# Kernel optimization log

Hardware: AMD Instinct MI355X
Metric: run time of the kernel (lower is better)

The kernel has to match this reference:

```python
import jax, jax.numpy as jnp
import numpy as np

B, L, E = 512, 64, 1024
D_MODEL, H = 1024, 16
HD = D_MODEL // H  # 64
SMOL_CH, SMOL_HID, SMOL_GEN = 32, 256, 256
LN_EPS = 1e-3


def _layernorm(x, g, b, eps=LN_EPS):
    m = jnp.mean(x, axis=-1, keepdims=True)
    v = jnp.mean(jnp.square(x - m), axis=-1, keepdims=True)
    return (x - m) * jax.lax.rsqrt(v + eps) * g + b


def setup_inputs() -> dict:
    key = jax.random.key(0)
    ks = jax.random.split(key, 12)
    s = lambda fan_in: 1.0 / np.sqrt(fan_in)
    inp = {
        'x': jax.random.normal(ks[0], (B, L, E), dtype=jnp.float32),
        # attention projections (stored as [in, out])
        'wq': jax.random.normal(ks[1], (E, D_MODEL), dtype=jnp.float32) * s(E),
        'bq': jnp.zeros((D_MODEL,), jnp.float32),
        'wk': jax.random.normal(ks[2], (E, D_MODEL), dtype=jnp.float32) * s(E),
        'bk': jnp.zeros((D_MODEL,), jnp.float32),
        'wv': jax.random.normal(ks[3], (E, D_MODEL), dtype=jnp.float32) * s(E),
        'bv': jnp.zeros((D_MODEL,), jnp.float32),
        'wo': jax.random.normal(ks[4], (D_MODEL, E), dtype=jnp.float32) * s(D_MODEL),
        'bo': jnp.zeros((E,), jnp.float32),
        # smolgen hypernetwork
        'sc_w': jax.random.normal(ks[5], (E, SMOL_CH), dtype=jnp.float32) * s(E),
        'sh1_w': jax.random.normal(ks[6], (L * SMOL_CH, SMOL_HID), dtype=jnp.float32) * s(L * SMOL_CH),
        'sh1_b': jnp.zeros((SMOL_HID,), jnp.float32),
        'ln1_g': jnp.ones((SMOL_HID,), jnp.float32),
        'ln1_b': jnp.zeros((SMOL_HID,), jnp.float32),
        'sg_w': jax.random.normal(ks[7], (SMOL_HID, H * SMOL_GEN), dtype=jnp.float32) * s(SMOL_HID),
        'sg_b': jnp.zeros((H * SMOL_GEN,), jnp.float32),
        'ln2_g': jnp.ones((H * SMOL_GEN,), jnp.float32),
        'ln2_b': jnp.zeros((H * SMOL_GEN,), jnp.float32),
        'swg_w': jax.random.normal(ks[8], (SMOL_GEN, L * L), dtype=jnp.float32) * s(SMOL_GEN),
    }
    return inp


def reference(x, wq, bq, wk, bk, wv, bv, wo, bo,
              sc_w, sh1_w, sh1_b, ln1_g, ln1_b,
              sg_w, sg_b, ln2_g, ln2_b, swg_w):
    b, l, _ = x.shape
    # q/k/v projections -> [b, h, l, hd]
    q = (x @ wq + bq).reshape(b, l, H, HD).transpose(0, 2, 1, 3)
    k = (x @ wk + bk).reshape(b, l, H, HD).transpose(0, 2, 1, 3)
    v = (x @ wv + bv).reshape(b, l, H, HD).transpose(0, 2, 1, 3)

    scale = jnp.sqrt(jnp.asarray(HD, x.dtype))
    attn_logits = jnp.einsum('bhqd,bhkd->bhqk', q, k) / scale  # [b,h,l,l]

    # smolgen: per-batch, per-head additive bias on the logits
    compressed = (x @ sc_w).reshape(b, l * SMOL_CH)            # [b, 2048]
    hidden = _layernorm(jax.nn.silu(compressed @ sh1_w + sh1_b), ln1_g, ln1_b)
    gen = _layernorm(jax.nn.silu(hidden @ sg_w + sg_b), ln2_g, ln2_b)
    gen = gen.reshape(b, H, SMOL_GEN)
    smol_w = (gen @ swg_w).reshape(b, H, l, l)
    attn_logits = attn_logits + smol_w

    # manual numerically-stable softmax (as in source)
    attn_logits = attn_logits - jnp.max(attn_logits, axis=-1, keepdims=True)
    attn_weights = jnp.exp(attn_logits)
    attn_weights = attn_weights / jnp.sum(attn_weights, axis=-1, keepdims=True)

    attn_output = jnp.einsum('bhqk,bhkd->bhqd', attn_weights, v)
    attn_output = attn_output.transpose(0, 2, 1, 3).reshape(b, l, D_MODEL)
    return attn_output @ wo + bo
```

## Files before the change

### kernel.cpp

```cpp
#include <hip/hip_runtime.h>
#include <hip/hip_bf16.h>

typedef unsigned short u16;
typedef __attribute__((ext_vector_type(8))) short short8;
typedef __attribute__((ext_vector_type(4))) float f32x4;
typedef const __attribute__((address_space(1))) void GV;
typedef __attribute__((address_space(3))) void LV;
#define GLOAD16(g, l) __builtin_amdgcn_global_load_lds((GV*)(g), (LV*)(l), 16, 0, 0)
#define BAR() asm volatile("s_barrier" ::: "memory")

#define BATCH 512
#define LSEQ  64
#define EMB   1024
#define NH    16
#define NQKV  3328
#define MROWS (BATCH*LSEQ)

__device__ __forceinline__ u16 f2b(float f){
  __hip_bfloat16 h = __float2bfloat16(f);
  return *reinterpret_cast<u16*>(&h);
}
__device__ __forceinline__ float b2f(u16 u){
  return __uint_as_float(((unsigned)u) << 16);
}
__device__ __forceinline__ uint2 pack4(float4 v){
  unsigned lo = (unsigned)f2b(v.x) | ((unsigned)f2b(v.y) << 16);
  unsigned hi = (unsigned)f2b(v.z) | ((unsigned)f2b(v.w) << 16);
  return make_uint2(lo, hi);
}

__device__ __forceinline__ void tpose(const float* __restrict__ src, u16* __restrict__ dst,
                                      int K, int N, int dstLd, int dstRowOff,
                                      int blk, int tid, float (*t)[33]){
  int nbx = N >> 5;
  int bx = blk % nbx, by = blk / nbx;
  int n0 = bx << 5, k0 = by << 5;
  int lx = tid & 31, ly = tid >> 5;
  #pragma unroll
  for (int i = 0; i < 32; i += 8)
    t[ly + i][lx] = src[(size_t)(k0 + ly + i) * N + n0 + lx];
  __syncthreads();
  #pragma unroll
  for (int i = 0; i < 32; i += 8)
    dst[(size_t)(dstRowOff + n0 + ly + i) * dstLd + k0 + lx] = f2b(t[lx][ly + i]);
}

#define PREP_BLOCKS 38157
__global__ __launch_bounds__(256) void prep_all(const float* __restrict__ x, u16* __restrict__ xb,
                                                const float* __restrict__ wq, const float* __restrict__ wk,
                                                const float* __restrict__ wv, const float* __restrict__ sc_w,
                                                const float* __restrict__ wo, const float* __restrict__ swg_w,
                                                u16* __restrict__ wqkvT, u16* __restrict__ woT,
                                                u16* __restrict__ swgT,
                                                const float* __restrict__ bq, const float* __restrict__ bk,
                                                const float* __restrict__ bv, float* __restrict__ qbias){
  __shared__ float t[32][33];
  const int blk = blockIdx.x, tid = threadIdx.x;
  if (blk < 32768){
    size_t i = ((size_t)blk * 256 + tid) * 4;
    float4 v = *(const float4*)&x[i];
    *(uint2*)&xb[i] = pack4(v);
  } else if (blk < 33792){
    tpose(wq,   wqkvT, 1024, 1024, 1024, 0,    blk - 32768, tid, t);
  } else if (blk < 34816){
    tpose(wk,   wqkvT, 1024, 1024, 1024, 1024, blk - 33792, tid, t);
  } else if (blk < 35840){
    tpose(wv,   wqkvT, 1024, 1024, 1024, 2048, blk - 34816, tid, t);
  } else if (blk < 35872){
    tpose(sc_w, wqkvT, 1024, 32,   1024, 3072, blk - 35840, tid, t);
  } else if (blk < 36896){
    tpose(wo,   woT,   1024, 1024, 1024, 0,    blk - 35872, tid, t);
  } else if (blk < 37920){
    tpose(swg_w, swgT, 256,  4096, 256,  0,    blk - 36896, tid, t);
  } else if (blk < 38144){
    size_t i = (size_t)(blk - 37920) * 1024 + tid * 4;
    *(uint2*)&wqkvT[(size_t)3104 * 1024 + i] = make_uint2(0, 0);
  } else {
    int i = (blk - 38144) * 256 + tid;
    if (i < NQKV){
      float v = 0.f;
      if (i < 1024) v = bq[i];
      else if (i < 2048) v = bk[i - 1024];
      else if (i < 3072) v = bv[i - 2048];
      qbias[i] = v;
    }
  }
}

template<int OUT_BF16, int HAS_BIAS>
__global__ __launch_bounds__(512, 2) void gemm256(const u16* __restrict__ A,
                                                  const u16* __restrict__ Bt,
                                                  const float* __restrict__ bias,
                                                  void* __restrict__ Cv,
                                                  int M, int N, int K){
  __shared__ u16 lA[2][16384];
  __shared__ u16 lB[2][16384];
  const int ntn = N >> 8;
  const int nwg = gridDim.x, bid = blockIdx.x;
  const int qq = nwg >> 3, r8 = nwg & 7, xcd = bid & 7, kk = bid >> 3;
  const int wg = (xcd < r8 ? xcd * (qq + 1) : r8 * (qq + 1) + (xcd - r8) * qq) + kk;
  const int tm = wg / ntn, tn = wg % ntn;
  const int m0 = tm << 8, n0 = tn << 8;
  const int tid = threadIdx.x;
  const int w = tid >> 6, lane = tid & 63;
  const int wm = w >> 2, wn = w & 3;
  const int l15 = lane & 15, l4 = lane >> 4;

  size_t ga[2][2], gb[2][2];
  #pragma unroll
  for (int j = 0; j < 2; j++){
    int ci = w * 128 + j * 64 + lane;
    int rh = ci >> 3, s = ci & 7;
    int gk = (s ^ (rh & 7)) * 8;
    #pragma unroll
    for (int h = 0; h < 2; h++){
      ga[h][j] = (size_t)(m0 + h * 128 + rh) * K + gk;
      gb[h][j] = (size_t)(n0 + h * 128 + rh) * K + gk;
    }
  }
  const int nk = K >> 6;

  auto stA = [&](int buf, int h, int kt){
    #pragma unroll
    for (int j = 0; j < 2; j++)
      GLOAD16(A + ga[h][j] + (size_t)kt * 64, &lA[buf][h * 8192 + (w * 128 + j * 64) * 8]);
  };
  auto stB = [&](int buf, int h, int kt){
    #pragma unroll
    for (int j = 0; j < 2; j++)
      GLOAD16(Bt + gb[h][j] + (size_t)kt * 64, &lB[buf][h * 8192 + (w * 128 + j * 64) * 8]);
  };

  stA(0, 0, 0); stB(0, 0, 0); stB(0, 1, 0); stA(0, 1, 0);
  stA(1, 0, 1); stB(1, 0, 1); stB(1, 1, 1);
  asm volatile("s_waitcnt vmcnt(6)" ::: "memory");
  BAR();

  f32x4 acc[8][4] = {};
  short8 a[4][2], b[4][2];

  for (int t = 0; t < nk; ++t){
    const int cur = t & 1;
    const u16* la = lA[cur];
    const u16* lb = lB[cur];

    #pragma unroll
    for (int f = 0; f < 4; f++){
      int r = f * 32 + wm * 16 + l15;
      #pragma unroll
      for (int ks = 0; ks < 2; ks++){
        int c = ks * 4 + l4;
        a[f][ks] = *(const short8*)&la[r * 64 + ((c ^ (r & 7)) * 8)];
      }
    }
    #pragma unroll
    for (int g = 0; g < 2; g++){
      int r = g * 64 + wn * 16 + l15;
      #pragma unroll
      for (int ks = 0; ks < 2; ks++){
        int c = ks * 4 + l4;
        b[g][ks] = *(const short8*)&lb[r * 64 + ((c ^ (r & 7)) * 8)];
      }
    }
    if (t + 1 < nk) stA(cur ^ 1, 1, t + 1);
    BAR();
    __builtin_amdgcn_s_setprio(1);
    #pragma unroll
    for (int f = 0; f < 4; f++)
      #pragma unroll
      for (int g = 0; g < 2; g++)
        #pragma unroll
        for (int ks = 0; ks < 2; ks++)
          acc[f][g] = __builtin_amdgcn_mfma_f32_16x16x32_bf16(a[f][ks], b[g][ks], acc[f][g], 0, 0, 0);
    __builtin_amdgcn_s_setprio(0);
    BAR();

    #pragma unroll
    for (int g = 2; g < 4; g++){
      int r = (g - 2) * 64 + wn * 16 + l15;
      #pragma unroll
      for (int ks = 0; ks < 2; ks++){
        int c = ks * 4 + l4;
        b[g][ks] = *(const short8*)&lb[8192 + r * 64 + ((c ^ (r & 7)) * 8)];
      }
    }
    if (t + 2 < nk) stA(cur, 0, t + 2);
    BAR();
    __builtin_amdgcn_s_setprio(1);
    #pragma unroll
    for (int f = 0; f < 4; f++)
      #pragma unroll
      for (int g = 2; g < 4; g++)
        #pragma unroll
        for (int ks = 0; ks < 2; ks++)
          acc[f][g] = __builtin_amdgcn_mfma_f32_16x16x32_bf16(a[f][ks], b[g][ks], acc[f][g], 0, 0, 0);
    __builtin_amdgcn_s_setprio(0);
    BAR();

    #pragma unroll
    for (int f = 0; f < 4; f++){
      int r = f * 32 + wm * 16 + l15;
      #pragma unroll
      for (int ks = 0; ks < 2; ks++){
        int c = ks * 4 + l4;
        a[f][ks] = *(const short8*)&la[8192 + r * 64 + ((c ^ (r & 7)) * 8)];
      }
    }
    if (t + 2 < nk) stB(cur, 0, t + 2);
    BAR();
    __builtin_amdgcn_s_setprio(1);
    #pragma unroll
    for (int f = 0; f < 4; f++)
      #pragma unroll
      for (int g = 2; g < 4; g++)
        #pragma unroll
        for (int ks = 0; ks < 2; ks++)
          acc[f + 4][g] = __builtin_amdgcn_mfma_f32_16x16x32_bf16(a[f][ks], b[g][ks], acc[f + 4][g], 0, 0, 0);
    __builtin_amdgcn_s_setprio(0);
    BAR();

    if (t + 2 < nk) stB(cur, 1, t + 2);
    if (t + 1 < nk){
      if (t + 2 < nk) asm volatile("s_waitcnt vmcnt(6)" ::: "memory");
      else            asm volatile("s_waitcnt vmcnt(0)" ::: "memory");
    }
    BAR();
    __builtin_amdgcn_s_setprio(1);
    #pragma unroll
    for (int f = 0; f < 4; f++)
      #pragma unroll
      for (int g = 0; g < 2; g++)
        #pragma unroll
        for (int ks = 0; ks < 2; ks++)
          acc[f + 4][g] = __builtin_amdgcn_mfma_f32_16x16x32_bf16(a[f][ks], b[g][ks], acc[f + 4][g], 0, 0, 0);
    __builtin_amdgcn_s_setprio(0);
    BAR();
  }

  #pragma unroll
  for (int f = 0; f < 8; f++){
    #pragma unroll
    for (int g = 0; g < 4; g++){
      int col = n0 + g * 64 + wn * 16 + l15;
      float bv = HAS_BIAS ? bias[col] : 0.0f;
      #pragma unroll
      for (int j = 0; j < 4; j++){
        int row = m0 + f * 32 + wm * 16 + l4 * 4 + j;
        float v = acc[f][g][j] + bv;
        if (OUT_BF16) ((u16*)Cv)[(size_t)row * N + col] = f2b(v);
        else          ((float*)Cv)[(size_t)row * N + col] = v;
      }
    }
  }
}

__global__ __launch_bounds__(512) void smol_hidden(const u16* __restrict__ qkvb,
                                                   const float* __restrict__ sh1_w,
                                                   const float* __restrict__ sh1_b,
                                                   const float* __restrict__ ln1_g,
                                                   const float* __restrict__ ln1_b,
                                                   float* __restrict__ hidden){
  const int b0 = blockIdx.x * 2;
  const int tid = threadIdx.x;
  __shared__ u16 cb[2][2048];
  __shared__ float part[8][2][256];
  __shared__ float rs[16];
  {
    int bi = tid >> 8, rem = tid & 255;
    int l = rem >> 2, cc = rem & 3;
    *(short8*)&cb[bi][rem * 8] =
        *(const short8*)&qkvb[(size_t)((b0 + bi) * 64 + l) * NQKV + 3072 + cc * 8];
  }
  __syncthreads();
  const int g = tid >> 6;
  const int c4 = (tid & 63) * 4;
  float4 a0 = {0,0,0,0}, a1 = {0,0,0,0};
  for (int kk2 = 0; kk2 < 256; kk2++){
    int k = g * 256 + kk2;
    float4 wv = *(const float4*)&sh1_w[(size_t)k * 256 + c4];
    float x0 = b2f(cb[0][k]), x1 = b2f(cb[1][k]);
    a0.x += x0 * wv.x; a0.y += x0 * wv.y; a0.z += x0 * wv.z; a0.w += x0 * wv.w;
    a1.x += x1 * wv.x; a1.y += x1 * wv.y; a1.z += x1 * wv.z; a1.w += x1 * wv.w;
  }
  *(float4*)&part[g][0][c4] = a0;
  *(float4*)&part[g][1][c4] = a1;
  __syncthreads();
  const int bi = tid >> 8, col = tid & 255;
  float y = sh1_b[col];
  #pragma unroll
  for (int g2 = 0; g2 < 8; g2++) y += part[g2][bi][col];
  y = y / (1.f + __expf(-y));
  float s = y, q = y * y;
  #pragma unroll
  for (int o = 32; o > 0; o >>= 1){ s += __shfl_down(s, o); q += __shfl_down(q, o); }
  int wv_ = tid >> 6;
  if ((tid & 63) == 0){ rs[wv_ * 2] = s; rs[wv_ * 2 + 1] = q; }
  __syncthreads();
  float S = 0, Q = 0;
  #pragma unroll
  for (int w2 = 0; w2 < 4; w2++){ S += rs[(bi * 4 + w2) * 2]; Q += rs[(bi * 4 + w2) * 2 + 1]; }
  float m = S * (1.f / 256.f), var = Q * (1.f / 256.f) - m * m;
  hidden[(size_t)(b0 + bi) * 256 + col] =
      (y - m) * rsqrtf(var + 1e-3f) * ln1_g[col] + ln1_b[col];
}

__global__ __launch_bounds__(512) void smol_gen(const float* __restrict__ hidden,
                                                const float* __restrict__ sg_w,
                                                const float* __restrict__ sg_b,
                                                const float* __restrict__ ln2_g,
                                                const float* __restrict__ ln2_b,
                                                u16* __restrict__ genb){
  const int b0 = blockIdx.x * 2;
  const int tid = threadIdx.x;
  __shared__ float hb[2][256];
  __shared__ float rs[32];
  if (tid < 512) hb[tid >> 8][tid & 255] = hidden[(size_t)(b0 + (tid >> 8)) * 256 + (tid & 255)];
  __syncthreads();
  const int c4 = tid * 4;
  float4 A00 = {0,0,0,0}, A01 = {0,0,0,0}, A10 = {0,0,0,0}, A11 = {0,0,0,0};
  for (int k = 0; k < 256; k++){
    float h0 = hb[0][k], h1 = hb[1][k];
    float4 w0 = *(const float4*)&sg_w[(size_t)k * 4096 + c4];
    float4 w1 = *(const float4*)&sg_w[(size_t)k * 4096 + 2048 + c4];
    A00.x += h0 * w0.x; A00.y += h0 * w0.y; A00.z += h0 * w0.z; A00.w += h0 * w0.w;
    A01.x += h0 * w1.x; A01.y += h0 * w1.y; A01.z += h0 * w1.z; A01.w += h0 * w1.w;
    A10.x += h1 * w0.x; A10.y += h1 * w0.y; A10.z += h1 * w0.z; A10.w += h1 * w0.w;
    A11.x += h1 * w1.x; A11.y += h1 * w1.y; A11.z += h1 * w1.z; A11.w += h1 * w1.w;
  }
  float4 b0v = *(const float4*)&sg_b[c4];
  float4 b1v = *(const float4*)&sg_b[2048 + c4];
  float s0 = 0, q0 = 0, s1 = 0, q1 = 0;
  float* p;
  #pragma unroll
  for (int e = 0; e < 4; e++){
    p = (float*)&A00; float y = p[e] + ((float*)&b0v)[e]; y = y / (1.f + __expf(-y)); p[e] = y; s0 += y; q0 += y * y;
    p = (float*)&A01; y = p[e] + ((float*)&b1v)[e]; y = y / (1.f + __expf(-y)); p[e] = y; s0 += y; q0 += y * y;
    p = (float*)&A10; y = p[e] + ((float*)&b0v)[e]; y = y / (1.f + __expf(-y)); p[e] = y; s1 += y; q1 += y * y;
    p = (float*)&A11; y = p[e] + ((float*)&b1v)[e]; y = y / (1.f + __expf(-y)); p[e] = y; s1 += y; q1 += y * y;
  }
  #pragma unroll
  for (int o = 32; o > 0; o >>= 1){
    s0 += __shfl_down(s0, o); q0 += __shfl_down(q0, o);
    s1 += __shfl_down(s1, o); q1 += __shfl_down(q1, o);
  }
  int wv_ = tid >> 6;
  if ((tid & 63) == 0){ rs[wv_ * 4] = s0; rs[wv_ * 4 + 1] = q0; rs[wv_ * 4 + 2] = s1; rs[wv_ * 4 + 3] = q1; }
  __syncthreads();
  float S0 = 0, Q0 = 0, S1 = 0, Q1 = 0;
  #pragma unroll
  for (int w2 = 0; w2 < 8; w2++){
    S0 += rs[w2 * 4]; Q0 += rs[w2 * 4 + 1]; S1 += rs[w2 * 4 + 2]; Q1 += rs[w2 * 4 + 3];
  }
  float m0 = S0 * (1.f / 4096.f), v0 = Q0 * (1.f / 4096.f) - m0 * m0;
  float m1 = S1 * (1.f / 4096.f), v1 = Q1 * (1.f / 4096.f) - m1 * m1;
  float is0 = rsqrtf(v0 + 1e-3f), is1 = rsqrtf(v1 + 1e-3f);
  float4 g0 = *(const float4*)&ln2_g[c4],        gb0 = *(const float4*)&ln2_b[c4];
  float4 g1 = *(const float4*)&ln2_g[2048 + c4], gb1 = *(const float4*)&ln2_b[2048 + c4];
  float4 o00, o01, o10, o11;
  #pragma unroll
  for (int e = 0; e < 4; e++){
    ((float*)&o00)[e] = (((float*)&A00)[e] - m0) * is0 * ((float*)&g0)[e] + ((float*)&gb0)[e];
    ((float*)&o01)[e] = (((float*)&A01)[e] - m0) * is0 * ((float*)&g1)[e] + ((float*)&gb1)[e];
    ((float*)&o10)[e] = (((float*)&A10)[e] - m1) * is1 * ((float*)&g0)[e] + ((float*)&gb0)[e];
    ((float*)&o11)[e] = (((float*)&A11)[e] - m1) * is1 * ((float*)&g1)[e] + ((float*)&gb1)[e];
  }
  *(uint2*)&genb[(size_t)(b0    ) * 4096 + c4]        = pack4(o00);
  *(uint2*)&genb[(size_t)(b0    ) * 4096 + 2048 + c4] = pack4(o01);
  *(uint2*)&genb[(size_t)(b0 + 1) * 4096 + c4]        = pack4(o10);
  *(uint2*)&genb[(size_t)(b0 + 1) * 4096 + 2048 + c4] = pack4(o11);
}

__global__ __launch_bounds__(256) void attn_fused(const u16* __restrict__ qkvb,
                                                  const float* __restrict__ smol,
                                                  u16* __restrict__ aout){
  const int bh = blockIdx.x;
  const int b = bh >> 4, h = bh & 15;
  __shared__ u16 qs[4096], kts[4096], vts[4096], ps[4096];
  __shared__ float Ss[64 * 68];
  const int tid = threadIdx.x, w = tid >> 6, lane = tid & 63;
  const int wm = w >> 1, wn = w & 1;

  const u16* qb = qkvb + (size_t)(b * 64) * NQKV + h * 64;
  const u16* kb = qb + 1024;
  const u16* vb = qb + 2048;

  #pragma unroll
  for (int i = 0; i < 2; i++){
    int c = i * 256 + tid;
    int r = c >> 3, cc = c & 7;
    int pc = cc ^ (r & 7);
    *(short8*)&qs [r * 64 + pc * 8] = *(const short8*)&qb[(size_t)r * NQKV + cc * 8];
    *(short8*)&kts[r * 64 + pc * 8] = *(const short8*)&kb[(size_t)r * NQKV + cc * 8];
    short8 vv = *(const short8*)&vb[(size_t)r * NQKV + cc * 8];
    #pragma unroll
    for (int j = 0; j < 8; j++){
      int hd = cc * 8 + j;
      int pcv = (r >> 3) ^ (hd & 7);
      vts[hd * 64 + pcv * 8 + (r & 7)] = (u16)vv[j];
    }
  }
  __syncthreads();

  f32x4 sacc[2][2] = {};
  #pragma unroll
  for (int ksi = 0; ksi < 2; ksi++){
    short8 af[2], bfr[2];
    #pragma unroll
    for (int f = 0; f < 2; f++){
      int ra = wm * 32 + f * 16 + (lane & 15);
      int ca = ksi * 4 + (lane >> 4);
      af[f]  = *(const short8*)&qs [ra * 64 + (ca ^ (ra & 7)) * 8];
      int rb = wn * 32 + f * 16 + (lane & 15);
      bfr[f] = *(const short8*)&kts[rb * 64 + (ca ^ (rb & 7)) * 8];
    }
    #pragma unroll
    for (int fm = 0; fm < 2; fm++)
      #pragma unroll
      for (int fn = 0; fn < 2; fn++)
        sacc[fm][fn] = __builtin_amdgcn_mfma_f32_16x16x32_bf16(af[fm], bfr[fn], sacc[fm][fn], 0, 0, 0);
  }
  const float* sm = smol + (size_t)bh * 4096;
  #pragma unroll
  for (int fm = 0; fm < 2; fm++)
    #pragma unroll
    for (int fn = 0; fn < 2; fn++)
      #pragma unroll
      for (int j = 0; j < 4; j++){
        int q  = wm * 32 + fm * 16 + (lane >> 4) * 4 + j;
        int kp = wn * 32 + fn * 16 + (lane & 15);
        Ss[q * 68 + kp] = sacc[fm][fn][j] * 0.125f + sm[q * 64 + kp];
      }
  __syncthreads();

  {
    int row = w * 16 + (lane >> 2);
    int sub = lane & 3;
    float* srow = &Ss[row * 68];
    float vals[16];
    float mx = -3.4e38f;
    #pragma unroll
    for (int i = 0; i < 16; i++){ vals[i] = srow[sub * 16 + i]; mx = fmaxf(mx, vals[i]); }
    mx = fmaxf(mx, __shfl_xor(mx, 1));
    mx = fmaxf(mx, __shfl_xor(mx, 2));
    float s = 0.f;
    #pragma unroll
    for (int i = 0; i < 16; i++){ vals[i] = __expf(vals[i] - mx); s += vals[i]; }
    s += __shfl_xor(s, 1);
    s += __shfl_xor(s, 2);
    float rinv = 1.f / s;
    short8 o0, o1;
    #pragma unroll
    for (int i = 0; i < 8; i++){ o0[i] = (short)f2b(vals[i] * rinv); o1[i] = (short)f2b(vals[8 + i] * rinv); }
    int c0 = sub * 2, c1 = sub * 2 + 1;
    *(short8*)&ps[row * 64 + (c0 ^ (row & 7)) * 8] = o0;
    *(short8*)&ps[row * 64 + (c1 ^ (row & 7)) * 8] = o1;
  }
  __syncthreads();

  f32x4 oacc[2][2] = {};
  #pragma unroll
  for (int ksi = 0; ksi < 2; ksi++){
    short8 af[2], bfr[2];
    #pragma unroll
    for (int f = 0; f < 2; f++){
      int ra = wm * 32 + f * 16 + (lane & 15);
      int ca = ksi * 4 + (lane >> 4);
      af[f]  = *(const short8*)&ps [ra * 64 + (ca ^ (ra & 7)) * 8];
      int rb = wn * 32 + f * 16 + (lane & 15);
      bfr[f] = *(const short8*)&vts[rb * 64 + (ca ^ (rb & 7)) * 8];
    }
    #pragma unroll
    for (int fm = 0; fm < 2; fm++)
      #pragma unroll
      for (int fn = 0; fn < 2; fn++)
        oacc[fm][fn] = __builtin_amdgcn_mfma_f32_16x16x32_bf16(af[fm], bfr[fn], oacc[fm][fn], 0, 0, 0);
  }
  #pragma unroll
  for (int fm = 0; fm < 2; fm++)
    #pragma unroll
    for (int fn = 0; fn < 2; fn++)
      #pragma unroll
      for (int j = 0; j < 4; j++){
        int q  = wm * 32 + fm * 16 + (lane >> 4) * 4 + j;
        int hd = wn * 32 + fn * 16 + (lane & 15);
        aout[(size_t)(b * 64 + q) * 1024 + h * 64 + hd] = f2b(oacc[fm][fn][j]);
      }
}

extern "C" void kernel_launch(void* const* d_in, const int* in_sizes, int n_in,
                              void* d_out, int out_size, void* d_ws, size_t ws_size,
                              hipStream_t stream){
  const float* x     = (const float*)d_in[0];
  const float* wq    = (const float*)d_in[1];
  const float* bq    = (const float*)d_in[2];
  const float* wk    = (const float*)d_in[3];
  const float* bk    = (const float*)d_in[4];
  const float* wv    = (const float*)d_in[5];
  const float* bv    = (const float*)d_in[6];
  const float* wo    = (const float*)d_in[7];
  const float* bo    = (const float*)d_in[8];
  const float* sc_w  = (const float*)d_in[9];
  const float* sh1_w = (const float*)d_in[10];
  const float* sh1_b = (const float*)d_in[11];
  const float* ln1_g = (const float*)d_in[12];
  const float* ln1_b = (const float*)d_in[13];
  const float* sg_w  = (const float*)d_in[14];
  const float* sg_b  = (const float*)d_in[15];
  const float* ln2_g = (const float*)d_in[16];
  const float* ln2_b = (const float*)d_in[17];
  const float* swg_w = (const float*)d_in[18];

  char* ws = (char*)d_ws;
  size_t off = 0;
  auto alloc = [&](size_t bytes){ void* p = ws + off; off += (bytes + 255) & ~(size_t)255; return p; };
  u16*   xb    = (u16*)  alloc((size_t)MROWS * EMB * 2);
  u16*   wqkvT = (u16*)  alloc((size_t)NQKV * EMB * 2);
  float* qbias = (float*)alloc((size_t)NQKV * 4);
  u16*   woT   = (u16*)  alloc((size_t)1024 * 1024 * 2);
  u16*   swgT  = (u16*)  alloc((size_t)4096 * 256 * 2);
  u16*   qkvb  = (u16*)  alloc((size_t)MROWS * NQKV * 2);
  float* hid   = (float*)alloc((size_t)512 * 256 * 4);
  u16*   genb  = (u16*)  alloc((size_t)512 * 4096 * 2);
  float* smol  = (float*)alloc((size_t)8192 * 4096 * 4);
  u16*   aout  = (u16*)  alloc((size_t)MROWS * 1024 * 2);

  prep_all<<<PREP_BLOCKS, 256, 0, stream>>>(x, xb, wq, wk, wv, sc_w, wo, swg_w,
                                            wqkvT, woT, swgT, bq, bk, bv, qbias);

  gemm256<1, 1><<<(MROWS / 256) * (NQKV / 256), 512, 0, stream>>>(
      xb, wqkvT, qbias, qkvb, MROWS, NQKV, 1024);

  smol_hidden<<<BATCH / 2, 512, 0, stream>>>(qkvb, sh1_w, sh1_b, ln1_g, ln1_b, hid);
  smol_gen   <<<BATCH / 2, 512, 0, stream>>>(hid, sg_w, sg_b, ln2_g, ln2_b, genb);
  gemm256<0, 0><<<(8192 / 256) * (4096 / 256), 512, 0, stream>>>(
      genb, swgT, nullptr, smol, 8192, 4096, 256);

  attn_fused<<<BATCH * NH, 256, 0, stream>>>(qkvb, smol, aout);

  gemm256<0, 1><<<(MROWS / 256) * (1024 / 256), 512, 0, stream>>>(
      aout, woT, bo, d_out, MROWS, 1024, 1024);
}
```

Before: 807.3 us.

## Store smolgen bias in bf16 and do softmax in registers per wave

The smolgen bias GEMM now writes bf16 instead of fp32, halving the 128MB intermediate write and its read in attention. The attention kernel is restructured so each wave owns 16 query rows across all 64 keys. The softmax is then done directly on MFMA accumulators with lane shuffles, which removes the fp32 LDS score buffer and one barrier. Rounding the bias to bf16 adds precision loss to the logits.

```diff
diff --git a/kernel.cpp b/kernel.cpp
--- a/kernel.cpp
+++ b/kernel.cpp
@@ -371,14 +371,13 @@
 }
 
 __global__ __launch_bounds__(256) void attn_fused(const u16* __restrict__ qkvb,
-                                                  const float* __restrict__ smol,
+                                                  const u16* __restrict__ smolb,
                                                   u16* __restrict__ aout){
   const int bh = blockIdx.x;
   const int b = bh >> 4, h = bh & 15;
   __shared__ u16 qs[4096], kts[4096], vts[4096], ps[4096];
-  __shared__ float Ss[64 * 68];
   const int tid = threadIdx.x, w = tid >> 6, lane = tid & 63;
-  const int wm = w >> 1, wn = w & 1;
+  const int l15 = lane & 15, g = lane >> 4;
 
   const u16* qb = qkvb + (size_t)(b * 64) * NQKV + h * 64;
   const u16* kb = qb + 1024;
@@ -401,90 +400,84 @@
   }
   __syncthreads();
 
-  f32x4 sacc[2][2] = {};
+  f32x4 sacc[4] = {};
   #pragma unroll
   for (int ksi = 0; ksi < 2; ksi++){
-    short8 af[2], bfr[2];
-    #pragma unroll
-    for (int f = 0; f < 2; f++){
-      int ra = wm * 32 + f * 16 + (lane & 15);
-      int ca = ksi * 4 + (lane >> 4);
-      af[f]  = *(const short8*)&qs [ra * 64 + (ca ^ (ra & 7)) * 8];
-      int rb = wn * 32 + f * 16 + (lane & 15);
-      bfr[f] = *(const short8*)&kts[rb * 64 + (ca ^ (rb & 7)) * 8];
-    }
-    #pragma unroll
-    for (int fm = 0; fm < 2; fm++)
-      #pragma unroll
-      for (int fn = 0; fn < 2; fn++)
-        sacc[fm][fn] = __builtin_amdgcn_mfma_f32_16x16x32_bf16(af[fm], bfr[fn], sacc[fm][fn], 0, 0, 0);
-  }
-  const float* sm = smol + (size_t)bh * 4096;
-  #pragma unroll
-  for (int fm = 0; fm < 2; fm++)
-    #pragma unroll
-    for (int fn = 0; fn < 2; fn++)
-      #pragma unroll
-      for (int j = 0; j < 4; j++){
-        int q  = wm * 32 + fm * 16 + (lane >> 4) * 4 + j;
-        int kp = wn * 32 + fn * 16 + (lane & 15);
-        Ss[q * 68 + kp] = sacc[fm][fn][j] * 0.125f + sm[q * 64 + kp];
-      }
-  __syncthreads();
-
-  {
-    int row = w * 16 + (lane >> 2);
-    int sub = lane & 3;
-    float* srow = &Ss[row * 68];
-    float vals[16];
-    float mx = -3.4e38f;
-    #pragma unroll
-    for (int i = 0; i < 16; i++){ vals[i] = srow[sub * 16 + i]; mx = fmaxf(mx, vals[i]); }
-    mx = fmaxf(mx, __shfl_xor(mx, 1));
-    mx = fmaxf(mx, __shfl_xor(mx, 2));
-    float s = 0.f;
-    #pragma unroll
-    for (int i = 0; i < 16; i++){ vals[i] = __expf(vals[i] - mx); s += vals[i]; }
-    s += __shfl_xor(s, 1);
-    s += __shfl_xor(s, 2);
-    float rinv = 1.f / s;
-    short8 o0, o1;
-    #pragma unroll
-    for (int i = 0; i < 8; i++){ o0[i] = (short)f2b(vals[i] * rinv); o1[i] = (short)f2b(vals[8 + i] * rinv); }
-    int c0 = sub * 2, c1 = sub * 2 + 1;
-    *(short8*)&ps[row * 64 + (c0 ^ (row & 7)) * 8] = o0;
-    *(short8*)&ps[row * 64 + (c1 ^ (row & 7)) * 8] = o1;
-  }
-  __syncthreads();
-
-  f32x4 oacc[2][2] = {};
+    int ra = w * 16 + l15;
+    int ca = ksi * 4 + g;
+    short8 af = *(const short8*)&qs[ra * 64 + ((ca ^ (ra & 7)) * 8)];
+    #pragma unroll
+    for (int fn = 0; fn < 4; fn++){
+      int rb = fn * 16 + l15;
+      short8 bf = *(const short8*)&kts[rb * 64 + ((ca ^ (rb & 7)) * 8)];
+      sacc[fn] = __builtin_amdgcn_mfma_f32_16x16x32_bf16(af, bf, sacc[fn], 0, 0, 0);
+    }
+  }
+
+  const u16* sm = smolb + (size_t)bh * 4096;
+  float vals[4][4];
+  float mx[4] = {-3.4e38f, -3.4e38f, -3.4e38f, -3.4e38f};
+  #pragma unroll
+  for (int fn = 0; fn < 4; fn++)
+    #pragma unroll
+    for (int j = 0; j < 4; j++){
+      int q = w * 16 + g * 4 + j;
+      float v = sacc[fn][j] * 0.125f + b2f(sm[q * 64 + fn * 16 + l15]);
+      vals[fn][j] = v;
+      mx[j] = fmaxf(mx[j], v);
+    }
+  #pragma unroll
+  for (int o = 1; o < 16; o <<= 1)
+    #pragma unroll
+    for (int j = 0; j < 4; j++) mx[j] = fmaxf(mx[j], __shfl_xor(mx[j], o));
+  float sum[4] = {0, 0, 0, 0};
+  #pragma unroll
+  for (int fn = 0; fn < 4; fn++)
+    #pragma unroll
+    for (int j = 0; j < 4; j++){
+      vals[fn][j] = __expf(vals[fn][j] - mx[j]);
+      sum[j] += vals[fn][j];
+    }
+  #pragma unroll
+  for (int o = 1; o < 16; o <<= 1)
+    #pragma unroll
+    for (int j = 0; j < 4; j++) sum[j] += __shfl_xor(sum[j], o);
+  float rinv[4];
+  #pragma unroll
+  for (int j = 0; j < 4; j++) rinv[j] = 1.f / sum[j];
+
+  #pragma unroll
+  for (int fn = 0; fn < 4; fn++)
+    #pragma unroll
+    for (int j = 0; j < 4; j++){
+      int q = w * 16 + g * 4 + j;
+      int c = fn * 16 + l15;
+      int cs = (c & 7) | ((((c >> 3) ^ (q & 7)) & 7) << 3);
+      ps[q * 64 + cs] = f2b(vals[fn][j] * rinv[j]);
+    }
+  __syncthreads();
+
+  f32x4 oacc[4] = {};
   #pragma unroll
   for (int ksi = 0; ksi < 2; ksi++){
-    short8 af[2], bfr[2];
-    #pragma unroll
-    for (int f = 0; f < 2; f++){
-      int ra = wm * 32 + f * 16 + (lane & 15);
-      int ca = ksi * 4 + (lane >> 4);
-      af[f]  = *(const short8*)&ps [ra * 64 + (ca ^ (ra & 7)) * 8];
-      int rb = wn * 32 + f * 16 + (lane & 15);
-      bfr[f] = *(const short8*)&vts[rb * 64 + (ca ^ (rb & 7)) * 8];
-    }
-    #pragma unroll
-    for (int fm = 0; fm < 2; fm++)
-      #pragma unroll
-      for (int fn = 0; fn < 2; fn++)
-        oacc[fm][fn] = __builtin_amdgcn_mfma_f32_16x16x32_bf16(af[fm], bfr[fn], oacc[fm][fn], 0, 0, 0);
-  }
-  #pragma unroll
-  for (int fm = 0; fm < 2; fm++)
-    #pragma unroll
-    for (int fn = 0; fn < 2; fn++)
-      #pragma unroll
-      for (int j = 0; j < 4; j++){
-        int q  = wm * 32 + fm * 16 + (lane >> 4) * 4 + j;
-        int hd = wn * 32 + fn * 16 + (lane & 15);
-        aout[(size_t)(b * 64 + q) * 1024 + h * 64 + hd] = f2b(oacc[fm][fn][j]);
-      }
+    int ra = w * 16 + l15;
+    int ca = ksi * 4 + g;
+    short8 af = *(const short8*)&ps[ra * 64 + ((ca ^ (ra & 7)) * 8)];
+    #pragma unroll
+    for (int fn = 0; fn < 4; fn++){
+      int rb = fn * 16 + l15;
+      short8 bf = *(const short8*)&vts[rb * 64 + ((ca ^ (rb & 7)) * 8)];
+      oacc[fn] = __builtin_amdgcn_mfma_f32_16x16x32_bf16(af, bf, oacc[fn], 0, 0, 0);
+    }
+  }
+  #pragma unroll
+  for (int fn = 0; fn < 4; fn++)
+    #pragma unroll
+    for (int j = 0; j < 4; j++){
+      int q  = w * 16 + g * 4 + j;
+      int hd = fn * 16 + l15;
+      aout[(size_t)(b * 64 + q) * 1024 + h * 64 + hd] = f2b(oacc[fn][j]);
+    }
 }
 
 extern "C" void kernel_launch(void* const* d_in, const int* in_sizes, int n_in,
@@ -521,7 +514,7 @@
   u16*   qkvb  = (u16*)  alloc((size_t)MROWS * NQKV * 2);
   float* hid   = (float*)alloc((size_t)512 * 256 * 4);
   u16*   genb  = (u16*)  alloc((size_t)512 * 4096 * 2);
-  float* smol  = (float*)alloc((size_t)8192 * 4096 * 4);
+  u16*   smolb = (u16*)  alloc((size_t)8192 * 4096 * 2);
   u16*   aout  = (u16*)  alloc((size_t)MROWS * 1024 * 2);
 
   prep_all<<<PREP_BLOCKS, 256, 0, stream>>>(x, xb, wq, wk, wv, sc_w, wo, swg_w,
@@ -532,10 +525,10 @@
 
   smol_hidden<<<BATCH / 2, 512, 0, stream>>>(qkvb, sh1_w, sh1_b, ln1_g, ln1_b, hid);
   smol_gen   <<<BATCH / 2, 512, 0, stream>>>(hid, sg_w, sg_b, ln2_g, ln2_b, genb);
-  gemm256<0, 0><<<(8192 / 256) * (4096 / 256), 512, 0, stream>>>(
-      genb, swgT, nullptr, smol, 8192, 4096, 256);
-
-  attn_fused<<<BATCH * NH, 256, 0, stream>>>(qkvb, smol, aout);
+  gemm256<1, 0><<<(8192 / 256) * (4096 / 256), 512, 0, stream>>>(
+      genb, swgT, nullptr, smolb, 8192, 4096, 256);
+
+  attn_fused<<<BATCH * NH, 256, 0, stream>>>(qkvb, smolb, aout);
 
   gemm256<0, 1><<<(MROWS / 256) * (1024 / 256), 512, 0, stream>>>(
       aout, woT, bo, d_out, MROWS, 1024, 1024);
```

After: 782.5 us. -3.1%, faster.
